# Optimization experiments

Measured on AMD Instinct MI355X. Metric: run time of the kernel, lower is better.

The kernel has to match this reference:

```python
import jax, jax.numpy as jnp
import numpy as np

B, T, N_EMBS, HEAD = 8, 2048, 1024, 64


def setup_inputs() -> dict:
    key = jax.random.key(0)
    k1, k2, k3, k4 = jax.random.split(key, 4)
    x = jax.random.normal(k1, (B, T, N_EMBS), dtype=jnp.float32)
    # nn.Linear(n_embs, head_size, bias=False): y = x @ W^T with W [head, n_embs].
    # We store the transposed weight [n_embs, head] directly for clean einsum.
    s = 1.0 / np.sqrt(N_EMBS)
    Wk = jax.random.uniform(k2, (N_EMBS, HEAD), jnp.float32, -s, s)
    Wq = jax.random.uniform(k3, (N_EMBS, HEAD), jnp.float32, -s, s)
    Wv = jax.random.uniform(k4, (N_EMBS, HEAD), jnp.float32, -s, s)
    return {"x": x, "Wk": Wk, "Wq": Wq, "Wv": Wv}


def reference(x, Wk, Wq, Wv):
    # Single causal self-attention head (dropout rate = 0.0).
    k = jnp.einsum("btn,nh->bth", x, Wk)  # [B,T,H]
    q = jnp.einsum("btn,nh->bth", x, Wq)
    v = jnp.einsum("btn,nh->bth", x, Wv)
    scale = k.shape[-1] ** -0.5
    scores = jnp.einsum("bqh,bkh->bqk", q, k) * scale  # [B,T,T]
    t = x.shape[1]
    causal = jnp.tril(jnp.ones((t, t), dtype=bool))
    scores = jnp.where(causal, scores, -jnp.inf)
    attn = jax.nn.softmax(scores, axis=-1)
    return jnp.einsum("bqk,bkh->bqh", attn, v)  # [B,T,H]
```

## Files before the change

### kernel.cpp

```cpp
#include <hip/hip_runtime.h>
#include <math.h>

#define BB 8
#define TT 2048
#define NE 1024
#define HH 64
#define BT (BB * TT)

typedef __attribute__((ext_vector_type(8))) short s8v;
typedef __attribute__((ext_vector_type(4))) float f4v;

__device__ inline unsigned short f2bf(float f) {
  union { float f; unsigned u; } v;
  v.f = f;
  unsigned r = (v.u + 0x7FFFu + ((v.u >> 16) & 1u)) >> 16;
  return (unsigned short)r;
}

__device__ inline unsigned short f2bf_trunc(float f) {
  union { float f; unsigned u; } v;
  v.f = f;
  return (unsigned short)(v.u >> 16);
}

__device__ inline unsigned cvtpk(float lo, float hi) {
  unsigned r;
  asm("v_cvt_pk_bf16_f32 %0, %1, %2" : "=v"(r) : "v"(lo), "v"(hi));
  return r;
}

__device__ inline void glds16(const unsigned short* g, unsigned short* l) {
  __builtin_amdgcn_global_load_lds(
      (const __attribute__((address_space(1))) unsigned*)g,
      (__attribute__((address_space(3))) unsigned*)l, 16, 0, 0);
}

__global__ __launch_bounds__(256) void conv_wt_kernel(
    const float* __restrict__ Wq, const float* __restrict__ Wk,
    const float* __restrict__ Wv, unsigned short* __restrict__ WTf) {
  const int idx = blockIdx.x * 256 + threadIdx.x;
  const int cb = idx >> 11;
  const int ks = (idx >> 6) & 31;
  const int lane = idx & 63;
  const int lr = lane & 15, lg = lane >> 4;
  const int col = cb * 16 + lr;
  const int m = col >> 6, h = col & 63;
  const int n0 = ks * 32 + lg * 8;
  const float* W = (m == 0) ? Wq : (m == 1) ? Wk : Wv;
  unsigned short v[8];
#pragma unroll
  for (int j = 0; j < 8; ++j) v[j] = f2bf(W[(size_t)(n0 + j) * HH + h]);
  *reinterpret_cast<uint4*>(WTf + (size_t)idx * 8) =
      *reinterpret_cast<const uint4*>(v);
}

__global__ __launch_bounds__(256, 5) void qkv_proj_mfma(
    const float* __restrict__ x, const unsigned short* __restrict__ WTf,
    unsigned short* __restrict__ Q, unsigned short* __restrict__ K,
    unsigned short* __restrict__ VT) {
  __shared__ __align__(16) unsigned short Bbuf[2][6144];
  __shared__ __align__(16) unsigned short Abuf[3][640];

  const int tid = threadIdx.x;
  const int lane = tid & 63;
  const int w = tid >> 6;
  const int lr = lane & 15, lg = lane >> 4;
  const int row0 = blockIdx.x * 16;

  const int arow = tid >> 4, aunit = tid & 15;
  const float* __restrict__ xsrc = x + (size_t)(row0 + arow) * NE + aunit * 2;

  f4v acc[3];
#pragma unroll
  for (int c = 0; c < 3; ++c) acc[c] = (f4v)0.f;

  float2 La[2];

  auto ISSUE_B = [&](int buf, int t) {
#pragma unroll
    for (int j = 0; j < 3; ++j) {
      const int cb = w * 3 + j;
      glds16(WTf + (size_t)(cb * 32 + t) * 512 + lane * 8, &Bbuf[buf][cb * 512]);
    }
  };

  La[0] = *reinterpret_cast<const float2*>(xsrc);
  La[1] = *reinterpret_cast<const float2*>(xsrc + 32);
  ISSUE_B(0, 0);
  *reinterpret_cast<unsigned*>(&Abuf[0][arow * 40 + aunit * 2]) =
      cvtpk(La[0].x, La[0].y);
  La[0] = *reinterpret_cast<const float2*>(xsrc + 2 * 32);
  *reinterpret_cast<unsigned*>(&Abuf[1][arow * 40 + aunit * 2]) =
      cvtpk(La[1].x, La[1].y);
  asm volatile("s_waitcnt vmcnt(1) lgkmcnt(0)" ::: "memory");
  __builtin_amdgcn_s_barrier();
  __builtin_amdgcn_sched_barrier(0);

#pragma unroll
  for (int t = 0; t < 32; ++t) {
    const int cur = t & 1;
    if (t + 1 < 32) ISSUE_B(cur ^ 1, t + 1);
    __builtin_amdgcn_sched_barrier(0);
    if (t + 3 < 32)
      La[(t + 3) & 1] = *reinterpret_cast<const float2*>(xsrc + (t + 3) * 32);
    __builtin_amdgcn_sched_barrier(0);
    const s8v a = *reinterpret_cast<const s8v*>(&Abuf[t % 3][lr * 40 + lg * 8]);
#pragma unroll
    for (int j = 0; j < 3; ++j) {
      const int cb = w * 3 + j;
      const s8v b = *reinterpret_cast<const s8v*>(&Bbuf[cur][cb * 512 + lane * 8]);
      acc[j] = __builtin_amdgcn_mfma_f32_16x16x32_bf16(a, b, acc[j], 0, 0, 0);
    }
    if (t + 2 < 32)
      *reinterpret_cast<unsigned*>(&Abuf[(t + 2) % 3][arow * 40 + aunit * 2]) =
          cvtpk(La[t & 1].x, La[t & 1].y);
    if (t + 1 < 32) {
      if (t + 3 < 32) {
        asm volatile("s_waitcnt vmcnt(1) lgkmcnt(0)" ::: "memory");
      } else {
        asm volatile("s_waitcnt vmcnt(0) lgkmcnt(0)" ::: "memory");
      }
      __builtin_amdgcn_s_barrier();
      __builtin_amdgcn_sched_barrier(0);
    }
  }

  const float QSCL = 0.18033688011112042f;
#pragma unroll
  for (int c = 0; c < 3; ++c) {
    const int col = (w * 3 + c) * 16 + lr;
    const int m = col >> 6;
    const int h = col & 63;
#pragma unroll
    for (int r = 0; r < 4; ++r) {
      const int rr = row0 + lg * 4 + r;
      if (m == 0) {
        Q[(size_t)rr * HH + h] = f2bf(acc[c][r] * QSCL);
      } else if (m == 1) {
        K[(size_t)rr * HH + h] = f2bf(acc[c][r]);
      } else {
        const int bb2 = rr >> 11, tt2 = rr & (TT - 1);
        VT[((size_t)bb2 * HH + h) * TT + tt2] = f2bf(acc[c][r]);
      }
    }
  }
}

__global__ __launch_bounds__(256, 3) void flash_attn_mfma(
    const unsigned short* __restrict__ Q, const unsigned short* __restrict__ K,
    const unsigned short* __restrict__ VT, float* __restrict__ out) {
  __shared__ unsigned short pl[4][16][72];
  __shared__ float ol[4][16][64];
  __shared__ float ml[4][16];
  __shared__ float ll[4][16];

  const int tid = threadIdx.x;
  const int lane = tid & 63;
  const int w = tid >> 6;
  const int lr = lane & 15;
  const int lg = lane >> 4;
  const int bid = blockIdx.x;
  const int b = bid & 7;
  const int qt = 127 - (bid >> 3);
  const int q0 = qt * 16;
  const size_t rowbase = (size_t)b * TT;

  const int nt = (qt >> 2) + 1;
  const int base = nt >> 2, rem = nt & 3;
  const int t0 = w * base + (w < rem ? w : rem);
  const int kend = t0 + base + (w < rem ? 1 : 0);

  const s8v qf0 = *reinterpret_cast<const s8v*>(
      Q + (rowbase + q0 + lr) * HH + lg * 8);
  const s8v qf1 = *reinterpret_cast<const s8v*>(
      Q + (rowbase + q0 + lr) * HH + 32 + lg * 8);

  s8v vone;
#pragma unroll
  for (int j = 0; j < 8; ++j) vone[j] = (short)0x3F80;

  f4v o[5];
#pragma unroll
  for (int n = 0; n < 5; ++n) o[n] = (f4v)0.f;
  float mrow[4];
#pragma unroll
  for (int r = 0; r < 4; ++r) mrow[r] = -INFINITY;

  const unsigned short* const Kb = K + rowbase * HH;

  s8v kfX[2][4], kfY[2][4];
  auto LOADK = [&](s8v (&kf)[2][4], int kt) {
    const int k0 = kt * 64;
#pragma unroll
    for (int nk = 0; nk < 4; ++nk) {
      const unsigned short* kp = Kb + (size_t)(k0 + 16 * nk + lr) * HH + lg * 8;
      kf[0][nk] = *reinterpret_cast<const s8v*>(kp);
      kf[1][nk] = *reinterpret_cast<const s8v*>(kp + 32);
    }
  };

  auto PROCESS = [&](const s8v (&kf)[2][4], int kt) {
    const int k0 = kt * 64;
    f4v s[4];
#pragma unroll
    for (int nk = 0; nk < 4; ++nk) s[nk] = (f4v)0.f;
    __builtin_amdgcn_s_setprio(1);
#pragma unroll
    for (int nk = 0; nk < 4; ++nk) {
      s[nk] = __builtin_amdgcn_mfma_f32_16x16x32_bf16(qf0, kf[0][nk], s[nk], 0, 0, 0);
      s[nk] = __builtin_amdgcn_mfma_f32_16x16x32_bf16(qf1, kf[1][nk], s[nk], 0, 0, 0);
    }
    __builtin_amdgcn_s_setprio(0);
    s8v vfr[2][4];
#pragma unroll
    for (int kh = 0; kh < 2; ++kh)
#pragma unroll
      for (int n = 0; n < 4; ++n)
        vfr[kh][n] = *reinterpret_cast<const s8v*>(
            VT + ((size_t)b * HH + 16 * n + lr) * TT + k0 + kh * 32 + lg * 8);

    if (kt == nt - 1) {
#pragma unroll
      for (int nk = 0; nk < 4; ++nk) {
        const int kk = k0 + 16 * nk + lr;
#pragma unroll
        for (int r = 0; r < 4; ++r) {
          const int qq = q0 + lg * 4 + r;
          if (kk > qq) s[nk][r] = -INFINITY;
        }
      }
    }

    float mx_[4];
    float grow = -INFINITY;
#pragma unroll
    for (int r = 0; r < 4; ++r) {
      float mx = fmaxf(fmaxf(s[0][r], s[1][r]), fmaxf(s[2][r], s[3][r]));
#pragma unroll
      for (int off = 1; off < 16; off <<= 1)
        mx = fmaxf(mx, __shfl_xor(mx, off));
      mx_[r] = mx;
      grow = fmaxf(grow, mx - mrow[r]);
    }
    if (!__all(grow <= 8.f)) {
#pragma unroll
      for (int r = 0; r < 4; ++r) {
        const float mnew = fmaxf(mrow[r], mx_[r]);
        const float scl = exp2f(mrow[r] - mnew);
        mrow[r] = mnew;
#pragma unroll
        for (int n = 0; n < 5; ++n) o[n][r] *= scl;
      }
    }
#pragma unroll
    for (int nk = 0; nk < 4; ++nk)
#pragma unroll
      for (int r = 0; r < 4; ++r)
        pl[w][lg * 4 + r][16 * nk + lr] = f2bf_trunc(exp2f(s[nk][r] - mrow[r]));
#pragma unroll
    for (int kh = 0; kh < 2; ++kh) {
      const int pc = kh * 32 + lg * 8;
      const ushort4 plo = *reinterpret_cast<const ushort4*>(&pl[w][lr][pc]);
      const ushort4 phi = *reinterpret_cast<const ushort4*>(&pl[w][lr][pc + 4]);
      s8v pa;
      pa[0] = plo.x; pa[1] = plo.y; pa[2] = plo.z; pa[3] = plo.w;
      pa[4] = phi.x; pa[5] = phi.y; pa[6] = phi.z; pa[7] = phi.w;
      __builtin_amdgcn_s_setprio(1);
#pragma unroll
      for (int n = 0; n < 4; ++n)
        o[n] = __builtin_amdgcn_mfma_f32_16x16x32_bf16(pa, vfr[kh][n], o[n], 0, 0, 0);
      o[4] = __builtin_amdgcn_mfma_f32_16x16x32_bf16(pa, vone, o[4], 0, 0, 0);
      __builtin_amdgcn_s_setprio(0);
    }
  };

  int kt = t0;
  if (kt < kend) LOADK(kfX, kt);
  while (kt + 2 <= kend) {
    LOADK(kfY, kt + 1);
    PROCESS(kfX, kt);
    if (kt + 2 < kend) LOADK(kfX, kt + 2);
    PROCESS(kfY, kt + 1);
    kt += 2;
  }
  if (kt < kend) PROCESS(kfX, kt);

#pragma unroll
  for (int n = 0; n < 4; ++n)
#pragma unroll
    for (int r = 0; r < 4; ++r) ol[w][lg * 4 + r][16 * n + lr] = o[n][r];
  if (lr == 0) {
#pragma unroll
    for (int r = 0; r < 4; ++r) {
      ml[w][lg * 4 + r] = mrow[r];
      ll[w][lg * 4 + r] = o[4][r];
    }
  }
  __syncthreads();

  const int row = tid >> 4;
  const int c0 = (tid & 15) * 4;
  float m0 = ml[0][row], m1 = ml[1][row], m2 = ml[2][row], m3 = ml[3][row];
  const float ms = fmaxf(fmaxf(m0, m1), fmaxf(m2, m3));
  const float w0 = exp2f(m0 - ms), w1 = exp2f(m1 - ms);
  const float w2 = exp2f(m2 - ms), w3 = exp2f(m3 - ms);
  const float lsum = w0 * ll[0][row] + w1 * ll[1][row] +
                     w2 * ll[2][row] + w3 * ll[3][row];
  float4 osum;
  osum.x = w0 * ol[0][row][c0 + 0] + w1 * ol[1][row][c0 + 0] +
           w2 * ol[2][row][c0 + 0] + w3 * ol[3][row][c0 + 0];
  osum.y = w0 * ol[0][row][c0 + 1] + w1 * ol[1][row][c0 + 1] +
           w2 * ol[2][row][c0 + 1] + w3 * ol[3][row][c0 + 1];
  osum.z = w0 * ol[0][row][c0 + 2] + w1 * ol[1][row][c0 + 2] +
           w2 * ol[2][row][c0 + 2] + w3 * ol[3][row][c0 + 2];
  osum.w = w0 * ol[0][row][c0 + 3] + w1 * ol[1][row][c0 + 3] +
           w2 * ol[2][row][c0 + 3] + w3 * ol[3][row][c0 + 3];
  const float inv = 1.0f / lsum;
  float4 res;
  res.x = osum.x * inv; res.y = osum.y * inv;
  res.z = osum.z * inv; res.w = osum.w * inv;
  *reinterpret_cast<float4*>(out + (rowbase + q0 + row) * HH + c0) = res;
}

extern "C" void kernel_launch(void* const* d_in, const int* in_sizes, int n_in,
                              void* d_out, int out_size, void* d_ws, size_t ws_size,
                              hipStream_t stream) {
  const float* x  = (const float*)d_in[0];
  const float* Wk = (const float*)d_in[1];
  const float* Wq = (const float*)d_in[2];
  const float* Wv = (const float*)d_in[3];
  float* out = (float*)d_out;

  unsigned short* ws = (unsigned short*)d_ws;
  unsigned short* Q  = ws;
  unsigned short* K  = ws + (size_t)BT * HH;
  unsigned short* VT = ws + 2 * (size_t)BT * HH;
  unsigned short* WT = ws + 3 * (size_t)BT * HH;

  conv_wt_kernel<<<96, 256, 0, stream>>>(Wq, Wk, Wv, WT);
  qkv_proj_mfma<<<1024, 256, 0, stream>>>(x, WT, Q, K, VT);
  flash_attn_mfma<<<1024, 256, 0, stream>>>(Q, K, VT, out);
}
```

Baseline: 76.16 us.

## Single-buffer K fragments and split V loads to raise attention occupancy

Replaces the two-tile unrolled double-buffered K fragment loop with a simple loop that prefetches the next K tile into one buffer after the QK MFMAs. V fragments are now loaded in two halves, the second half issued just before it is needed, and a scheduling barrier is added. Launch bounds go from 3 to 4 blocks per SIMD to exploit the lower register pressure. The cost is that each load gets less lead time to hide latency within a wave, which the extra resident waves are meant to cover.

```diff
diff --git a/kernel.cpp b/kernel.cpp
--- a/kernel.cpp
+++ b/kernel.cpp
@@ -146,7 +146,7 @@
   }
 }
 
-__global__ __launch_bounds__(256, 3) void flash_attn_mfma(
+__global__ __launch_bounds__(256, 4) void flash_attn_mfma(
     const unsigned short* __restrict__ Q, const unsigned short* __restrict__ K,
     const unsigned short* __restrict__ VT, float* __restrict__ out) {
   __shared__ unsigned short pl[4][16][72];
@@ -187,9 +187,10 @@
   for (int r = 0; r < 4; ++r) mrow[r] = -INFINITY;
 
   const unsigned short* const Kb = K + rowbase * HH;
-
-  s8v kfX[2][4], kfY[2][4];
-  auto LOADK = [&](s8v (&kf)[2][4], int kt) {
+  const unsigned short* const Vb = VT + (size_t)b * HH * TT;
+
+  s8v kf[2][4];
+  auto LOADK = [&](int kt) {
     const int k0 = kt * 64;
 #pragma unroll
     for (int nk = 0; nk < 4; ++nk) {
@@ -199,7 +200,8 @@
     }
   };
 
-  auto PROCESS = [&](const s8v (&kf)[2][4], int kt) {
+  if (t0 < kend) LOADK(t0);
+  for (int kt = t0; kt < kend; ++kt) {
     const int k0 = kt * 64;
     f4v s[4];
 #pragma unroll
@@ -211,13 +213,13 @@
       s[nk] = __builtin_amdgcn_mfma_f32_16x16x32_bf16(qf1, kf[1][nk], s[nk], 0, 0, 0);
     }
     __builtin_amdgcn_s_setprio(0);
-    s8v vfr[2][4];
-#pragma unroll
-    for (int kh = 0; kh < 2; ++kh)
-#pragma unroll
-      for (int n = 0; n < 4; ++n)
-        vfr[kh][n] = *reinterpret_cast<const s8v*>(
-            VT + ((size_t)b * HH + 16 * n + lr) * TT + k0 + kh * 32 + lg * 8);
+    if (kt + 1 < kend) LOADK(kt + 1);
+    s8v vfr0[4];
+#pragma unroll
+    for (int n = 0; n < 4; ++n)
+      vfr0[n] = *reinterpret_cast<const s8v*>(
+          Vb + (size_t)(16 * n + lr) * TT + k0 + lg * 8);
+    __builtin_amdgcn_sched_barrier(0);
 
     if (kt == nt - 1) {
 #pragma unroll
@@ -257,33 +259,39 @@
 #pragma unroll
       for (int r = 0; r < 4; ++r)
         pl[w][lg * 4 + r][16 * nk + lr] = f2bf_trunc(exp2f(s[nk][r] - mrow[r]));
-#pragma unroll
-    for (int kh = 0; kh < 2; ++kh) {
-      const int pc = kh * 32 + lg * 8;
-      const ushort4 plo = *reinterpret_cast<const ushort4*>(&pl[w][lr][pc]);
-      const ushort4 phi = *reinterpret_cast<const ushort4*>(&pl[w][lr][pc + 4]);
+
+    {
+      const ushort4 plo = *reinterpret_cast<const ushort4*>(&pl[w][lr][lg * 8]);
+      const ushort4 phi = *reinterpret_cast<const ushort4*>(&pl[w][lr][lg * 8 + 4]);
       s8v pa;
       pa[0] = plo.x; pa[1] = plo.y; pa[2] = plo.z; pa[3] = plo.w;
       pa[4] = phi.x; pa[5] = phi.y; pa[6] = phi.z; pa[7] = phi.w;
+      s8v vfr1[4];
+#pragma unroll
+      for (int n = 0; n < 4; ++n)
+        vfr1[n] = *reinterpret_cast<const s8v*>(
+            Vb + (size_t)(16 * n + lr) * TT + k0 + 32 + lg * 8);
       __builtin_amdgcn_s_setprio(1);
 #pragma unroll
       for (int n = 0; n < 4; ++n)
-        o[n] = __builtin_amdgcn_mfma_f32_16x16x32_bf16(pa, vfr[kh][n], o[n], 0, 0, 0);
+        o[n] = __builtin_amdgcn_mfma_f32_16x16x32_bf16(pa, vfr0[n], o[n], 0, 0, 0);
       o[4] = __builtin_amdgcn_mfma_f32_16x16x32_bf16(pa, vone, o[4], 0, 0, 0);
       __builtin_amdgcn_s_setprio(0);
-    }
-  };
-
-  int kt = t0;
-  if (kt < kend) LOADK(kfX, kt);
-  while (kt + 2 <= kend) {
-    LOADK(kfY, kt + 1);
-    PROCESS(kfX, kt);
-    if (kt + 2 < kend) LOADK(kfX, kt + 2);
-    PROCESS(kfY, kt + 1);
-    kt += 2;
+      const ushort4 qlo =
+          *reinterpret_cast<const ushort4*>(&pl[w][lr][32 + lg * 8]);
+      const ushort4 qhi =
+          *reinterpret_cast<const ushort4*>(&pl[w][lr][32 + lg * 8 + 4]);
+      s8v pb;
+      pb[0] = qlo.x; pb[1] = qlo.y; pb[2] = qlo.z; pb[3] = qlo.w;
+      pb[4] = qhi.x; pb[5] = qhi.y; pb[6] = qhi.z; pb[7] = qhi.w;
+      __builtin_amdgcn_s_setprio(1);
+#pragma unroll
+      for (int n = 0; n < 4; ++n)
+        o[n] = __builtin_amdgcn_mfma_f32_16x16x32_bf16(pb, vfr1[n], o[n], 0, 0, 0);
+      o[4] = __builtin_amdgcn_mfma_f32_16x16x32_bf16(pb, vone, o[4], 0, 0, 0);
+      __builtin_amdgcn_s_setprio(0);
+    }
   }
-  if (kt < kend) PROCESS(kfX, kt);
 
 #pragma unroll
   for (int n = 0; n < 4; ++n)
```

Result: slower. 77.74 us (+2.1%).

## Single-buffer K loads, raise occupancy, and defer row-max shuffles to rescale path

Applied to the files above, without the earlier changes.

Replaces the two-register-set K double buffer with a single buffer whose next-tile load is issued right after the QK MFMAs. Launch bounds are raised to 4 blocks per CU to use the freed registers. The per-tile cross-lane max shuffle reduction now runs only when some lane's local max exceeds the running max by the threshold, removing shuffles from the common path. Prefetch distance is shorter, so load latency is hidden by occupancy instead of by buffering.

```diff
diff --git a/kernel.cpp b/kernel.cpp
--- a/kernel.cpp
+++ b/kernel.cpp
@@ -146,7 +146,7 @@
   }
 }
 
-__global__ __launch_bounds__(256, 3) void flash_attn_mfma(
+__global__ __launch_bounds__(256, 4) void flash_attn_mfma(
     const unsigned short* __restrict__ Q, const unsigned short* __restrict__ K,
     const unsigned short* __restrict__ VT, float* __restrict__ out) {
   __shared__ unsigned short pl[4][16][72];
@@ -187,9 +187,10 @@
   for (int r = 0; r < 4; ++r) mrow[r] = -INFINITY;
 
   const unsigned short* const Kb = K + rowbase * HH;
-
-  s8v kfX[2][4], kfY[2][4];
-  auto LOADK = [&](s8v (&kf)[2][4], int kt) {
+  const unsigned short* const Vb = VT + (size_t)b * HH * TT;
+
+  s8v kf[2][4];
+  auto LOADK = [&](int kt) {
     const int k0 = kt * 64;
 #pragma unroll
     for (int nk = 0; nk < 4; ++nk) {
@@ -199,7 +200,8 @@
     }
   };
 
-  auto PROCESS = [&](const s8v (&kf)[2][4], int kt) {
+  if (t0 < kend) LOADK(t0);
+  for (int kt = t0; kt < kend; ++kt) {
     const int k0 = kt * 64;
     f4v s[4];
 #pragma unroll
@@ -211,13 +213,15 @@
       s[nk] = __builtin_amdgcn_mfma_f32_16x16x32_bf16(qf1, kf[1][nk], s[nk], 0, 0, 0);
     }
     __builtin_amdgcn_s_setprio(0);
+    if (kt + 1 < kend) LOADK(kt + 1);
     s8v vfr[2][4];
 #pragma unroll
     for (int kh = 0; kh < 2; ++kh)
 #pragma unroll
       for (int n = 0; n < 4; ++n)
         vfr[kh][n] = *reinterpret_cast<const s8v*>(
-            VT + ((size_t)b * HH + 16 * n + lr) * TT + k0 + kh * 32 + lg * 8);
+            Vb + (size_t)(16 * n + lr) * TT + k0 + kh * 32 + lg * 8);
+    __builtin_amdgcn_sched_barrier(0);
 
     if (kt == nt - 1) {
 #pragma unroll
@@ -231,21 +235,21 @@
       }
     }
 
-    float mx_[4];
-    float grow = -INFINITY;
-#pragma unroll
-    for (int r = 0; r < 4; ++r) {
-      float mx = fmaxf(fmaxf(s[0][r], s[1][r]), fmaxf(s[2][r], s[3][r]));
-#pragma unroll
-      for (int off = 1; off < 16; off <<= 1)
-        mx = fmaxf(mx, __shfl_xor(mx, off));
-      mx_[r] = mx;
-      grow = fmaxf(grow, mx - mrow[r]);
-    }
-    if (!__all(grow <= 8.f)) {
+    float lmax[4];
+#pragma unroll
+    for (int r = 0; r < 4; ++r)
+      lmax[r] = fmaxf(fmaxf(s[0][r], s[1][r]), fmaxf(s[2][r], s[3][r]));
+    bool ok = true;
+#pragma unroll
+    for (int r = 0; r < 4; ++r) ok = ok && (lmax[r] - mrow[r] <= 8.f);
+    if (!__all(ok)) {
 #pragma unroll
       for (int r = 0; r < 4; ++r) {
-        const float mnew = fmaxf(mrow[r], mx_[r]);
+        float mx = lmax[r];
+#pragma unroll
+        for (int off = 1; off < 16; off <<= 1)
+          mx = fmaxf(mx, __shfl_xor(mx, off));
+        const float mnew = fmaxf(mrow[r], mx);
         const float scl = exp2f(mrow[r] - mnew);
         mrow[r] = mnew;
 #pragma unroll
@@ -257,6 +261,7 @@
 #pragma unroll
       for (int r = 0; r < 4; ++r)
         pl[w][lg * 4 + r][16 * nk + lr] = f2bf_trunc(exp2f(s[nk][r] - mrow[r]));
+
 #pragma unroll
     for (int kh = 0; kh < 2; ++kh) {
       const int pc = kh * 32 + lg * 8;
@@ -272,18 +277,7 @@
       o[4] = __builtin_amdgcn_mfma_f32_16x16x32_bf16(pa, vone, o[4], 0, 0, 0);
       __builtin_amdgcn_s_setprio(0);
     }
-  };
-
-  int kt = t0;
-  if (kt < kend) LOADK(kfX, kt);
-  while (kt + 2 <= kend) {
-    LOADK(kfY, kt + 1);
-    PROCESS(kfX, kt);
-    if (kt + 2 < kend) LOADK(kfX, kt + 2);
-    PROCESS(kfY, kt + 1);
-    kt += 2;
   }
-  if (kt < kend) PROCESS(kfX, kt);
 
 #pragma unroll
   for (int n = 0; n < 4; ++n)
```

Measured after the change: 86.57 us. 1.14x slower.

## Drop K double-buffering and ones-MFMA row sum to raise occupancy to 4

Applied to the files above, without the earlier changes.

Removes the register double-buffered K fragment prefetch and loads K inline inside a simple loop. It replaces the extra MFMA against a ones vector, which computed the softmax denominator, with a shuffle-reduced row sum in registers. Launch bounds go from 3 to 4 waves per SIMD. The aim is to cut register pressure so more waves are resident and can hide latency, at the cost of losing explicit load prefetch and adding cross-lane shuffles per tile.

```diff
diff --git a/kernel.cpp b/kernel.cpp
--- a/kernel.cpp
+++ b/kernel.cpp
@@ -146,7 +146,7 @@
   }
 }
 
-__global__ __launch_bounds__(256, 3) void flash_attn_mfma(
+__global__ __launch_bounds__(256, 4) void flash_attn_mfma(
     const unsigned short* __restrict__ Q, const unsigned short* __restrict__ K,
     const unsigned short* __restrict__ VT, float* __restrict__ out) {
   __shared__ unsigned short pl[4][16][72];
@@ -168,38 +168,21 @@
   const int nt = (qt >> 2) + 1;
   const int base = nt >> 2, rem = nt & 3;
   const int t0 = w * base + (w < rem ? w : rem);
-  const int kend = t0 + base + (w < rem ? 1 : 0);
+  const int cnt = base + (w < rem ? 1 : 0);
 
   const s8v qf0 = *reinterpret_cast<const s8v*>(
       Q + (rowbase + q0 + lr) * HH + lg * 8);
   const s8v qf1 = *reinterpret_cast<const s8v*>(
       Q + (rowbase + q0 + lr) * HH + 32 + lg * 8);
 
-  s8v vone;
-#pragma unroll
-  for (int j = 0; j < 8; ++j) vone[j] = (short)0x3F80;
-
-  f4v o[5];
-#pragma unroll
-  for (int n = 0; n < 5; ++n) o[n] = (f4v)0.f;
-  float mrow[4];
-#pragma unroll
-  for (int r = 0; r < 4; ++r) mrow[r] = -INFINITY;
-
-  const unsigned short* const Kb = K + rowbase * HH;
-
-  s8v kfX[2][4], kfY[2][4];
-  auto LOADK = [&](s8v (&kf)[2][4], int kt) {
-    const int k0 = kt * 64;
-#pragma unroll
-    for (int nk = 0; nk < 4; ++nk) {
-      const unsigned short* kp = Kb + (size_t)(k0 + 16 * nk + lr) * HH + lg * 8;
-      kf[0][nk] = *reinterpret_cast<const s8v*>(kp);
-      kf[1][nk] = *reinterpret_cast<const s8v*>(kp + 32);
-    }
-  };
-
-  auto PROCESS = [&](const s8v (&kf)[2][4], int kt) {
+  f4v o[4];
+#pragma unroll
+  for (int n = 0; n < 4; ++n) o[n] = (f4v)0.f;
+  float mrow[4], lrow[4];
+#pragma unroll
+  for (int r = 0; r < 4; ++r) { mrow[r] = -INFINITY; lrow[r] = 0.f; }
+
+  for (int kt = t0; kt < t0 + cnt; ++kt) {
     const int k0 = kt * 64;
     f4v s[4];
 #pragma unroll
@@ -207,8 +190,11 @@
     __builtin_amdgcn_s_setprio(1);
 #pragma unroll
     for (int nk = 0; nk < 4; ++nk) {
-      s[nk] = __builtin_amdgcn_mfma_f32_16x16x32_bf16(qf0, kf[0][nk], s[nk], 0, 0, 0);
-      s[nk] = __builtin_amdgcn_mfma_f32_16x16x32_bf16(qf1, kf[1][nk], s[nk], 0, 0, 0);
+      const unsigned short* kp = K + (rowbase + k0 + 16 * nk + lr) * HH + lg * 8;
+      const s8v kf0 = *reinterpret_cast<const s8v*>(kp);
+      const s8v kf1 = *reinterpret_cast<const s8v*>(kp + 32);
+      s[nk] = __builtin_amdgcn_mfma_f32_16x16x32_bf16(qf0, kf0, s[nk], 0, 0, 0);
+      s[nk] = __builtin_amdgcn_mfma_f32_16x16x32_bf16(qf1, kf1, s[nk], 0, 0, 0);
     }
     __builtin_amdgcn_s_setprio(0);
     s8v vfr[2][4];
@@ -248,15 +234,30 @@
         const float mnew = fmaxf(mrow[r], mx_[r]);
         const float scl = exp2f(mrow[r] - mnew);
         mrow[r] = mnew;
-#pragma unroll
-        for (int n = 0; n < 5; ++n) o[n][r] *= scl;
-      }
+        lrow[r] *= scl;
+#pragma unroll
+        for (int n = 0; n < 4; ++n) o[n][r] *= scl;
+      }
+    }
+#pragma unroll
+    for (int r = 0; r < 4; ++r) {
+      float rs = 0.f;
+#pragma unroll
+      for (int nk = 0; nk < 4; ++nk) {
+        const float p = exp2f(s[nk][r] - mrow[r]);
+        s[nk][r] = p;
+        rs += p;
+      }
+#pragma unroll
+      for (int off = 1; off < 16; off <<= 1)
+        rs += __shfl_xor(rs, off);
+      lrow[r] += rs;
     }
 #pragma unroll
     for (int nk = 0; nk < 4; ++nk)
 #pragma unroll
       for (int r = 0; r < 4; ++r)
-        pl[w][lg * 4 + r][16 * nk + lr] = f2bf_trunc(exp2f(s[nk][r] - mrow[r]));
+        pl[w][lg * 4 + r][16 * nk + lr] = f2bf_trunc(s[nk][r]);
 #pragma unroll
     for (int kh = 0; kh < 2; ++kh) {
       const int pc = kh * 32 + lg * 8;
@@ -269,21 +270,9 @@
 #pragma unroll
       for (int n = 0; n < 4; ++n)
         o[n] = __builtin_amdgcn_mfma_f32_16x16x32_bf16(pa, vfr[kh][n], o[n], 0, 0, 0);
-      o[4] = __builtin_amdgcn_mfma_f32_16x16x32_bf16(pa, vone, o[4], 0, 0, 0);
       __builtin_amdgcn_s_setprio(0);
     }
-  };
-
-  int kt = t0;
-  if (kt < kend) LOADK(kfX, kt);
-  while (kt + 2 <= kend) {
-    LOADK(kfY, kt + 1);
-    PROCESS(kfX, kt);
-    if (kt + 2 < kend) LOADK(kfX, kt + 2);
-    PROCESS(kfY, kt + 1);
-    kt += 2;
   }
-  if (kt < kend) PROCESS(kfX, kt);
 
 #pragma unroll
   for (int n = 0; n < 4; ++n)
@@ -293,7 +282,7 @@
 #pragma unroll
     for (int r = 0; r < 4; ++r) {
       ml[w][lg * 4 + r] = mrow[r];
-      ll[w][lg * 4 + r] = o[4][r];
+      ll[w][lg * 4 + r] = lrow[r];
     }
   }
   __syncthreads();
```

New measurement: 71.30 us. 6.4% less time.
